# Kernel optimization log

Measured on AMD Instinct MI355X. Metric: run time of the kernel, lower is better.

The kernel has to match this reference:

```python
import jax, jax.numpy as jnp
import numpy as np

N, E = 50000, 800000
DIN, DH, DOUT = 128, 64, 16


def setup_inputs() -> dict:
    key = jax.random.key(0)
    ks = jax.random.split(key, 8)
    s = lambda d: np.float32(1.0 / np.sqrt(d))
    return {
        "x": jax.random.normal(ks[0], (N, DIN), jnp.float32),
        "edge_index": jax.random.randint(ks[1], (2, E), 0, N, dtype=jnp.int32),
        "w0": jax.random.normal(ks[2], (DIN, DH), jnp.float32) * s(DIN),
        "b0": jnp.zeros((DH,), jnp.float32),
        "w1": jax.random.normal(ks[3], (DH, DH), jnp.float32) * s(DH),
        "b1": jnp.zeros((DH,), jnp.float32),
        "w2": jax.random.normal(ks[4], (DH, DH), jnp.float32) * s(DH),
        "b2": jnp.zeros((DH,), jnp.float32),
        "fc_w": jax.random.normal(ks[5], (DH, DOUT), jnp.float32) * s(DH),
        "fc_b": jnp.zeros((DOUT,), jnp.float32),
    }


def reference(x, edge_index, w0, b0, w1, b1, w2, b2, fc_w, fc_b):
    n = x.shape[0]
    loop = jnp.arange(n, dtype=edge_index.dtype)
    # PyG GCNConv default: add self-loops, symmetric normalization
    src = jnp.concatenate([edge_index[0], loop])  # [E+N]
    dst = jnp.concatenate([edge_index[1], loop])
    deg = jax.ops.segment_sum(jnp.ones_like(dst, dtype=x.dtype), dst, num_segments=n)
    dinv = jnp.where(deg > 0, jax.lax.rsqrt(deg), 0.0)
    norm = dinv[src] * dinv[dst]  # [E+N]

    def conv(h, W, b):
        h = h @ W                            # [N, DH]
        msg = h[src] * norm[:, None]         # [E+N, DH] gather + scale
        return jax.ops.segment_sum(msg, dst, num_segments=n) + b

    h = jax.nn.elu(conv(x, w0, b0))
    h = jax.nn.elu(conv(h, w1, b1))
    h = jax.nn.elu(conv(h, w2, b2))
    return jax.nn.softmax(h @ fc_w + fc_b, axis=1)
```

## Files before the change

kernel.cpp:

```cpp
#include <hip/hip_runtime.h>
#include <hip/hip_fp16.h>
#include <math.h>

#define NWIN 8

typedef _Float16 f16x8 __attribute__((ext_vector_type(8)));
typedef float f32x4 __attribute__((ext_vector_type(4)));

__device__ __forceinline__ float eluf(float v) { return v > 0.f ? v : expm1f(v); }

__global__ __launch_bounds__(256) void deg_kernel(const int* __restrict__ dst,
                                                  int* __restrict__ counts, int E) {
    int e = blockIdx.x * 256 + threadIdx.x;
    if (e < E) atomicAdd(&counts[dst[e]], 1);
}

__global__ __launch_bounds__(256) void alloc_kernel(const int* __restrict__ counts,
                                                    int* __restrict__ gtotal,
                                                    int* __restrict__ offs,
                                                    int* __restrict__ cursor,
                                                    float* __restrict__ dinv, int n) {
    int i = blockIdx.x * 256 + threadIdx.x;
    if (i >= n) return;
    int c = counts[i];
    int pad = (c + 7) & ~7;
    int o = atomicAdd(gtotal, pad);
    offs[i] = o;
    cursor[i] = o;
    dinv[i] = rsqrtf((float)(c + 1));
}

__global__ __launch_bounds__(256) void fill_kernel(int* __restrict__ a, int v, int cap) {
    int i = blockIdx.x * 256 + threadIdx.x;
    if (i < cap) a[i] = v;
}

__global__ __launch_bounds__(256) void scatter_kernel(const int* __restrict__ src,
                                                      const int* __restrict__ dst,
                                                      int* __restrict__ cursor,
                                                      int* __restrict__ csr_src,
                                                      int E, int winSize) {
    int win = blockIdx.x & (NWIN - 1);
    int group = blockIdx.x >> 3;
    int nGroups = gridDim.x >> 3;
    int lo = win * winSize, hi = lo + winSize;
    int stride = nGroups * 256;
    for (int e = group * 256 + threadIdx.x; e < E; e += stride) {
        int d = dst[e];
        if (d >= lo && d < hi) {
            int j = atomicAdd(&cursor[d], 1);
            csr_src[j] = src[e];
        }
    }
}

__global__ __launch_bounds__(256) void mm128_mfma(const float* __restrict__ H,
                                                  const float* __restrict__ W,
                                                  const float* __restrict__ dinv,
                                                  __half* __restrict__ TA,
                                                  __half* __restrict__ TB,
                                                  int n, int nTiles) {
    __shared__ _Float16 bhi[4][4][64][8];
    __shared__ _Float16 blo[4][4][64][8];
    int tid = threadIdx.x;
    for (int it = 0; it < 32; ++it) {
        int idx = it * 256 + tid;
        int k = idx >> 6, nn = idx & 63;
        float w = W[idx];
        _Float16 h = (_Float16)w;
        _Float16 l = (_Float16)(w - (float)h);
        int kt = k >> 5, kr = k & 31;
        int g = kr >> 3, j = kr & 7;
        int ct = nn >> 4, c = nn & 15;
        bhi[kt][ct][g * 16 + c][j] = h;
        blo[kt][ct][g * 16 + c][j] = l;
    }
    if (blockIdx.x == 0 && tid < 32) {
        TA[n * 32 + tid] = __float2half(0.f);
        TB[n * 32 + tid] = __float2half(0.f);
    }
    __syncthreads();

    int wave = blockIdx.x * 4 + (tid >> 6);
    if (wave >= nTiles) return;
    int lane = tid & 63;
    f16x8 Bh[4][4], Bl[4][4];
    #pragma unroll
    for (int kt = 0; kt < 4; ++kt)
        #pragma unroll
        for (int ct = 0; ct < 4; ++ct) {
            Bh[kt][ct] = *(const f16x8*)&bhi[kt][ct][lane][0];
            Bl[kt][ct] = *(const f16x8*)&blo[kt][ct][lane][0];
        }
    int row0 = wave * 16;
    int arow = row0 + (lane & 15);
    if (arow >= n) arow = n - 1;
    const float* hp = H + (size_t)arow * 128 + ((lane >> 4) << 3);
    f32x4 acc[4];
    #pragma unroll
    for (int ct = 0; ct < 4; ++ct) acc[ct] = (f32x4){0.f, 0.f, 0.f, 0.f};
    #pragma unroll
    for (int kt = 0; kt < 4; ++kt) {
        float4 p0 = *(const float4*)(hp + kt * 32);
        float4 p1 = *(const float4*)(hp + kt * 32 + 4);
        float v[8] = {p0.x, p0.y, p0.z, p0.w, p1.x, p1.y, p1.z, p1.w};
        f16x8 ah, al;
        #pragma unroll
        for (int j = 0; j < 8; ++j) {
            _Float16 h = (_Float16)v[j];
            ah[j] = h;
            al[j] = (_Float16)(v[j] - (float)h);
        }
        #pragma unroll
        for (int ct = 0; ct < 4; ++ct) {
            acc[ct] = __builtin_amdgcn_mfma_f32_16x16x32_f16(ah, Bh[kt][ct], acc[ct], 0, 0, 0);
            acc[ct] = __builtin_amdgcn_mfma_f32_16x16x32_f16(al, Bh[kt][ct], acc[ct], 0, 0, 0);
            acc[ct] = __builtin_amdgcn_mfma_f32_16x16x32_f16(ah, Bl[kt][ct], acc[ct], 0, 0, 0);
        }
    }
    int rbase = row0 + ((lane >> 4) << 2);
    int cbase = lane & 15;
    #pragma unroll
    for (int r = 0; r < 4; ++r) {
        int row = rbase + r;
        if (row < n) {
            float d = dinv[row];
            #pragma unroll
            for (int ct = 0; ct < 4; ++ct) {
                int col = ct * 16 + cbase;
                __half* P = (col < 32) ? TA : TB;
                P[row * 32 + (col & 31)] = __float2half(acc[ct][r] * d);
            }
        }
    }
}

__global__ __launch_bounds__(256) void gatherA_kernel(const __half* __restrict__ P,
                                                      const int* __restrict__ offs,
                                                      const int* __restrict__ cnt,
                                                      const int* __restrict__ csr_src,
                                                      float* __restrict__ agg, int n) {
    int t = blockIdx.x * 256 + threadIdx.x;
    int node = t >> 4, l = t & 15;
    if (node >= n) return;
    const __half2* P2 = (const __half2*)P;
    float2 sv = __half22float2(P2[node * 16 + l]);
    float ax0 = sv.x, ay0 = sv.y;
    float ax1 = 0, ay1 = 0, ax2 = 0, ay2 = 0, ax3 = 0, ay3 = 0;
    int e0 = offs[node];
    int e1 = e0 + ((cnt[node] + 7) & ~7);
    #pragma unroll 1
    for (int e = e0; e < e1; e += 8) {
        int s0 = __builtin_nontemporal_load(csr_src + e);
        int s1 = __builtin_nontemporal_load(csr_src + e + 1);
        int s2 = __builtin_nontemporal_load(csr_src + e + 2);
        int s3 = __builtin_nontemporal_load(csr_src + e + 3);
        int s4 = __builtin_nontemporal_load(csr_src + e + 4);
        int s5 = __builtin_nontemporal_load(csr_src + e + 5);
        int s6 = __builtin_nontemporal_load(csr_src + e + 6);
        int s7 = __builtin_nontemporal_load(csr_src + e + 7);
        float2 v0 = __half22float2(P2[s0 * 16 + l]);
        float2 v1 = __half22float2(P2[s1 * 16 + l]);
        float2 v2 = __half22float2(P2[s2 * 16 + l]);
        float2 v3 = __half22float2(P2[s3 * 16 + l]);
        float2 v4 = __half22float2(P2[s4 * 16 + l]);
        float2 v5 = __half22float2(P2[s5 * 16 + l]);
        float2 v6 = __half22float2(P2[s6 * 16 + l]);
        float2 v7 = __half22float2(P2[s7 * 16 + l]);
        ax0 += v0.x + v4.x;  ay0 += v0.y + v4.y;
        ax1 += v1.x + v5.x;  ay1 += v1.y + v5.y;
        ax2 += v2.x + v6.x;  ay2 += v2.y + v6.y;
        ax3 += v3.x + v7.x;  ay3 += v3.y + v7.y;
    }
    float rx = (ax0 + ax1) + (ax2 + ax3);
    float ry = (ay0 + ay1) + (ay2 + ay3);
    __builtin_nontemporal_store(rx, agg + node * 32 + 2 * l);
    __builtin_nontemporal_store(ry, agg + node * 32 + 2 * l + 1);
}

__global__ __launch_bounds__(256, 4) void gatherB_mm(const __half* __restrict__ PB,
                                                     const float* __restrict__ agg,
                                                     const int* __restrict__ offs,
                                                     const int* __restrict__ cnt,
                                                     const int* __restrict__ csr_src,
                                                     const float* __restrict__ dinv,
                                                     const float* __restrict__ bias,
                                                     const float* __restrict__ Wn,
                                                     __half* __restrict__ outA,
                                                     __half* __restrict__ outB, int n) {
    __shared__ _Float16 bhi[2][4][64][8];
    __shared__ _Float16 blo[2][4][64][8];
    __shared__ float rowbuf[64][68];
    int tid = threadIdx.x;
    for (int it = 0; it < 16; ++it) {
        int idx = it * 256 + tid;
        int k = idx >> 6, nn = idx & 63;
        float w = Wn[idx];
        _Float16 h = (_Float16)w;
        _Float16 lo = (_Float16)(w - (float)h);
        int kt = k >> 5, kr = k & 31;
        int g = kr >> 3, j = kr & 7;
        int ct = nn >> 4, c = nn & 15;
        bhi[kt][ct][g * 16 + c][j] = h;
        blo[kt][ct][g * 16 + c][j] = lo;
    }
    if (blockIdx.x == 0 && tid < 32) {
        outA[n * 32 + tid] = __float2half(0.f);
        outB[n * 32 + tid] = __float2half(0.f);
    }
    int g16 = tid >> 4, l = tid & 15;
    int nodebase = blockIdx.x * 64;
    const __half2* P2 = (const __half2*)PB;
    #pragma unroll 1
    for (int q = 0; q < 4; ++q) {
        int ln = 4 * g16 + q;
        int node = nodebase + ln;
        float h0 = 0.f, h1 = 0.f, h2 = 0.f, h3 = 0.f;
        if (node < n) {
            float2 sv = __half22float2(P2[node * 16 + l]);
            float ax0 = sv.x, ay0 = sv.y;
            float ax1 = 0, ay1 = 0, ax2 = 0, ay2 = 0, ax3 = 0, ay3 = 0;
            int e0 = offs[node];
            int e1 = e0 + ((cnt[node] + 7) & ~7);
            #pragma unroll 1
            for (int e = e0; e < e1; e += 8) {
                int s0 = __builtin_nontemporal_load(csr_src + e);
                int s1 = __builtin_nontemporal_load(csr_src + e + 1);
                int s2 = __builtin_nontemporal_load(csr_src + e + 2);
                int s3 = __builtin_nontemporal_load(csr_src + e + 3);
                int s4 = __builtin_nontemporal_load(csr_src + e + 4);
                int s5 = __builtin_nontemporal_load(csr_src + e + 5);
                int s6 = __builtin_nontemporal_load(csr_src + e + 6);
                int s7 = __builtin_nontemporal_load(csr_src + e + 7);
                float2 v0 = __half22float2(P2[s0 * 16 + l]);
                float2 v1 = __half22float2(P2[s1 * 16 + l]);
                float2 v2 = __half22float2(P2[s2 * 16 + l]);
                float2 v3 = __half22float2(P2[s3 * 16 + l]);
                float2 v4 = __half22float2(P2[s4 * 16 + l]);
                float2 v5 = __half22float2(P2[s5 * 16 + l]);
                float2 v6 = __half22float2(P2[s6 * 16 + l]);
                float2 v7 = __half22float2(P2[s7 * 16 + l]);
                ax0 += v0.x + v4.x;  ay0 += v0.y + v4.y;
                ax1 += v1.x + v5.x;  ay1 += v1.y + v5.y;
                ax2 += v2.x + v6.x;  ay2 += v2.y + v6.y;
                ax3 += v3.x + v7.x;  ay3 += v3.y + v7.y;
            }
            float shx = (ax0 + ax1) + (ax2 + ax3);
            float shy = (ay0 + ay1) + (ay2 + ay3);
            float a0 = __builtin_nontemporal_load(agg + node * 32 + 2 * l);
            float a1 = __builtin_nontemporal_load(agg + node * 32 + 2 * l + 1);
            float di = dinv[node];
            float2 bl = *(const float2*)(bias + 2 * l);
            float2 bh = *(const float2*)(bias + 32 + 2 * l);
            h0 = eluf(a0 * di + bl.x);
            h1 = eluf(a1 * di + bl.y);
            h2 = eluf(shx * di + bh.x);
            h3 = eluf(shy * di + bh.y);
        }
        *(float2*)&rowbuf[ln][2 * l] = make_float2(h0, h1);
        *(float2*)&rowbuf[ln][32 + 2 * l] = make_float2(h2, h3);
    }
    __syncthreads();

    int wv = tid >> 6, lane = tid & 63;
    f16x8 Bh[2][4], Bl[2][4];
    #pragma unroll
    for (int kt = 0; kt < 2; ++kt)
        #pragma unroll
        for (int ct = 0; ct < 4; ++ct) {
            Bh[kt][ct] = *(const f16x8*)&bhi[kt][ct][lane][0];
            Bl[kt][ct] = *(const f16x8*)&blo[kt][ct][lane][0];
        }
    int trow = wv * 16 + (lane & 15);
    int kb = (lane >> 4) << 3;
    f32x4 acc[4];
    #pragma unroll
    for (int ct = 0; ct < 4; ++ct) acc[ct] = (f32x4){0.f, 0.f, 0.f, 0.f};
    #pragma unroll
    for (int kt = 0; kt < 2; ++kt) {
        float4 p0 = *(const float4*)&rowbuf[trow][kt * 32 + kb];
        float4 p1 = *(const float4*)&rowbuf[trow][kt * 32 + kb + 4];
        float v[8] = {p0.x, p0.y, p0.z, p0.w, p1.x, p1.y, p1.z, p1.w};
        f16x8 ah, al;
        #pragma unroll
        for (int j = 0; j < 8; ++j) {
            _Float16 h = (_Float16)v[j];
            ah[j] = h;
            al[j] = (_Float16)(v[j] - (float)h);
        }
        #pragma unroll
        for (int ct = 0; ct < 4; ++ct) {
            acc[ct] = __builtin_amdgcn_mfma_f32_16x16x32_f16(ah, Bh[kt][ct], acc[ct], 0, 0, 0);
            acc[ct] = __builtin_amdgcn_mfma_f32_16x16x32_f16(al, Bh[kt][ct], acc[ct], 0, 0, 0);
            acc[ct] = __builtin_amdgcn_mfma_f32_16x16x32_f16(ah, Bl[kt][ct], acc[ct], 0, 0, 0);
        }
    }
    int rb = wv * 16 + ((lane >> 4) << 2);
    int cb = lane & 15;
    #pragma unroll
    for (int r = 0; r < 4; ++r) {
        int node = nodebase + rb + r;
        if (node < n) {
            float d = dinv[node];
            #pragma unroll
            for (int ct = 0; ct < 4; ++ct) {
                int col = ct * 16 + cb;
                __half* P = (col < 32) ? outA : outB;
                P[node * 32 + (col & 31)] = __float2half(acc[ct][r] * d);
            }
        }
    }
}

__global__ __launch_bounds__(256, 4) void gatherB_fc(const __half* __restrict__ PB,
                                                     const float* __restrict__ agg,
                                                     const int* __restrict__ offs,
                                                     const int* __restrict__ cnt,
                                                     const int* __restrict__ csr_src,
                                                     const float* __restrict__ dinv,
                                                     const float* __restrict__ bias,
                                                     const float* __restrict__ fcw,
                                                     const float* __restrict__ fcb,
                                                     float* __restrict__ out, int n) {
    __shared__ _Float16 bhi[2][64][8];
    __shared__ _Float16 blo[2][64][8];
    __shared__ float rowbuf[64][68];
    int tid = threadIdx.x;
    for (int it = 0; it < 4; ++it) {
        int idx = it * 256 + tid;
        int k = idx >> 4, j16 = idx & 15;
        float w = fcw[idx];
        _Float16 h = (_Float16)w;
        _Float16 lo = (_Float16)(w - (float)h);
        int kt = k >> 5, kr = k & 31;
        int g = kr >> 3, j = kr & 7;
        bhi[kt][g * 16 + j16][j] = h;
        blo[kt][g * 16 + j16][j] = lo;
    }
    int g16 = tid >> 4, l = tid & 15;
    int nodebase = blockIdx.x * 64;
    const __half2* P2 = (const __half2*)PB;
    #pragma unroll 1
    for (int q = 0; q < 4; ++q) {
        int ln = 4 * g16 + q;
        int node = nodebase + ln;
        float h0 = 0.f, h1 = 0.f, h2 = 0.f, h3 = 0.f;
        if (node < n) {
            float2 sv = __half22float2(P2[node * 16 + l]);
            float ax0 = sv.x, ay0 = sv.y;
            float ax1 = 0, ay1 = 0, ax2 = 0, ay2 = 0, ax3 = 0, ay3 = 0;
            int e0 = offs[node];
            int e1 = e0 + ((cnt[node] + 7) & ~7);
            #pragma unroll 1
            for (int e = e0; e < e1; e += 8) {
                int s0 = __builtin_nontemporal_load(csr_src + e);
                int s1 = __builtin_nontemporal_load(csr_src + e + 1);
                int s2 = __builtin_nontemporal_load(csr_src + e + 2);
                int s3 = __builtin_nontemporal_load(csr_src + e + 3);
                int s4 = __builtin_nontemporal_load(csr_src + e + 4);
                int s5 = __builtin_nontemporal_load(csr_src + e + 5);
                int s6 = __builtin_nontemporal_load(csr_src + e + 6);
                int s7 = __builtin_nontemporal_load(csr_src + e + 7);
                float2 v0 = __half22float2(P2[s0 * 16 + l]);
                float2 v1 = __half22float2(P2[s1 * 16 + l]);
                float2 v2 = __half22float2(P2[s2 * 16 + l]);
                float2 v3 = __half22float2(P2[s3 * 16 + l]);
                float2 v4 = __half22float2(P2[s4 * 16 + l]);
                float2 v5 = __half22float2(P2[s5 * 16 + l]);
                float2 v6 = __half22float2(P2[s6 * 16 + l]);
                float2 v7 = __half22float2(P2[s7 * 16 + l]);
                ax0 += v0.x + v4.x;  ay0 += v0.y + v4.y;
                ax1 += v1.x + v5.x;  ay1 += v1.y + v5.y;
                ax2 += v2.x + v6.x;  ay2 += v2.y + v6.y;
                ax3 += v3.x + v7.x;  ay3 += v3.y + v7.y;
            }
            float shx = (ax0 + ax1) + (ax2 + ax3);
            float shy = (ay0 + ay1) + (ay2 + ay3);
            float a0 = __builtin_nontemporal_load(agg + node * 32 + 2 * l);
            float a1 = __builtin_nontemporal_load(agg + node * 32 + 2 * l + 1);
            float di = dinv[node];
            float2 bl = *(const float2*)(bias + 2 * l);
            float2 bh = *(const float2*)(bias + 32 + 2 * l);
            h0 = eluf(a0 * di + bl.x);
            h1 = eluf(a1 * di + bl.y);
            h2 = eluf(shx * di + bh.x);
            h3 = eluf(shy * di + bh.y);
        }
        *(float2*)&rowbuf[ln][2 * l] = make_float2(h0, h1);
        *(float2*)&rowbuf[ln][32 + 2 * l] = make_float2(h2, h3);
    }
    __syncthreads();

    int wv = tid >> 6, lane = tid & 63;
    f16x8 Bh[2], Bl[2];
    #pragma unroll
    for (int kt = 0; kt < 2; ++kt) {
        Bh[kt] = *(const f16x8*)&bhi[kt][lane][0];
        Bl[kt] = *(const f16x8*)&blo[kt][lane][0];
    }
    int trow = wv * 16 + (lane & 15);
    int kb = (lane >> 4) << 3;
    f32x4 acc = (f32x4){0.f, 0.f, 0.f, 0.f};
    #pragma unroll
    for (int kt = 0; kt < 2; ++kt) {
        float4 p0 = *(const float4*)&rowbuf[trow][kt * 32 + kb];
        float4 p1 = *(const float4*)&rowbuf[trow][kt * 32 + kb + 4];
        float v[8] = {p0.x, p0.y, p0.z, p0.w, p1.x, p1.y, p1.z, p1.w};
        f16x8 ah, al;
        #pragma unroll
        for (int j = 0; j < 8; ++j) {
            _Float16 h = (_Float16)v[j];
            ah[j] = h;
            al[j] = (_Float16)(v[j] - (float)h);
        }
        acc = __builtin_amdgcn_mfma_f32_16x16x32_f16(ah, Bh[kt], acc, 0, 0, 0);
        acc = __builtin_amdgcn_mfma_f32_16x16x32_f16(al, Bh[kt], acc, 0, 0, 0);
        acc = __builtin_amdgcn_mfma_f32_16x16x32_f16(ah, Bl[kt], acc, 0, 0, 0);
    }
    float bj = fcb[lane & 15];
    #pragma unroll
    for (int r = 0; r < 4; ++r) {
        float o = acc[r] + bj;
        float m = o;
        #pragma unroll
        for (int d = 8; d; d >>= 1) m = fmaxf(m, __shfl_xor(m, d, 64));
        float ex = expf(o - m);
        float s = ex;
        #pragma unroll
        for (int d = 8; d; d >>= 1) s += __shfl_xor(s, d, 64);
        int node = nodebase + wv * 16 + ((lane >> 4) << 2) + r;
        if (node < n) out[(size_t)node * 16 + (lane & 15)] = ex / s;
    }
}

extern "C" void kernel_launch(void* const* d_in, const int* in_sizes, int n_in,
                              void* d_out, int out_size, void* d_ws, size_t ws_size,
                              hipStream_t stream) {
    const float* x   = (const float*)d_in[0];
    const int*   ei  = (const int*)d_in[1];
    const float* w0  = (const float*)d_in[2];
    const float* b0  = (const float*)d_in[3];
    const float* w1  = (const float*)d_in[4];
    const float* b1  = (const float*)d_in[5];
    const float* w2  = (const float*)d_in[6];
    const float* b2  = (const float*)d_in[7];
    const float* fcw = (const float*)d_in[8];
    const float* fcb = (const float*)d_in[9];
    float* out = (float*)d_out;

    const int N = in_sizes[0] / 128;
    const int E = in_sizes[1] / 2;
    const int* src = ei;
    const int* dst = ei + E;
    const int csr_cap = E + 8 * N + 8;

    char* p = (char*)d_ws;
    auto take = [&](size_t bytes) {
        char* q = p;
        p += (bytes + 255) & ~(size_t)255;
        return q;
    };
    int*    counts  = (int*)take((size_t)(N + 1) * 4);
    int*    gtotal  = counts + N;
    int*    offs    = (int*)take((size_t)N * 4);
    int*    cursor  = (int*)take((size_t)N * 4);
    float*  dinv    = (float*)take((size_t)N * 4);
    int*    csr_src = (int*)take((size_t)csr_cap * 4);
    float*  aggbuf  = (float*)take((size_t)N * 32 * 4);
    __half* TA0     = (__half*)take((size_t)(N + 1) * 32 * 2);
    __half* TB0     = (__half*)take((size_t)(N + 1) * 32 * 2);
    __half* TA1     = (__half*)take((size_t)(N + 1) * 32 * 2);
    __half* TB1     = (__half*)take((size_t)(N + 1) * 32 * 2);

    hipMemsetAsync(counts, 0, (size_t)(N + 1) * 4, stream);

    deg_kernel<<<(E + 255) / 256, 256, 0, stream>>>(dst, counts, E);
    alloc_kernel<<<(N + 255) / 256, 256, 0, stream>>>(counts, gtotal, offs, cursor, dinv, N);
    fill_kernel<<<(csr_cap + 255) / 256, 256, 0, stream>>>(csr_src, N, csr_cap);
    int winSize = (N + NWIN - 1) / NWIN;
    scatter_kernel<<<1024, 256, 0, stream>>>(src, dst, cursor, csr_src, E, winSize);

    int nTiles = (N + 15) / 16;
    int gA_grid = (N + 15) / 16;
    int gB_grid = (N + 63) / 64;

    mm128_mfma<<<(nTiles + 3) / 4, 256, 0, stream>>>(x, w0, dinv, TA0, TB0, N, nTiles);

    gatherA_kernel<<<gA_grid, 256, 0, stream>>>(TA0, offs, counts, csr_src, aggbuf, N);
    gatherB_mm<<<gB_grid, 256, 0, stream>>>(TB0, aggbuf, offs, counts, csr_src,
                                            dinv, b0, w1, TA1, TB1, N);
    gatherA_kernel<<<gA_grid, 256, 0, stream>>>(TA1, offs, counts, csr_src, aggbuf, N);
    gatherB_mm<<<gB_grid, 256, 0, stream>>>(TB1, aggbuf, offs, counts, csr_src,
                                            dinv, b1, w2, TA0, TB0, N);
    gatherA_kernel<<<gA_grid, 256, 0, stream>>>(TA0, offs, counts, csr_src, aggbuf, N);
    gatherB_fc<<<gB_grid, 256, 0, stream>>>(TB0, aggbuf, offs, counts, csr_src,
                                            dinv, b2, fcw, fcb, out, N);
}
```

Baseline: 306.7 us.

## Fuse split-half gathers into single 64-wide aggregation kernel with 16-byte loads

```diff
diff --git a/kernel.cpp b/kernel.cpp
--- a/kernel.cpp
+++ b/kernel.cpp
@@ -6,8 +6,15 @@
 
 typedef _Float16 f16x8 __attribute__((ext_vector_type(8)));
 typedef float f32x4 __attribute__((ext_vector_type(4)));
+typedef int i32x4 __attribute__((ext_vector_type(4)));
+typedef unsigned int u32x4 __attribute__((ext_vector_type(4)));
 
 __device__ __forceinline__ float eluf(float v) { return v > 0.f ? v : expm1f(v); }
+
+__device__ __forceinline__ float2 cvt2(unsigned int w) {
+    __half2 h = *reinterpret_cast<const __half2*>(&w);
+    return __half22float2(h);
+}
 
 __global__ __launch_bounds__(256) void deg_kernel(const int* __restrict__ dst,
                                                   int* __restrict__ counts, int E) {
@@ -19,7 +26,8 @@
                                                     int* __restrict__ gtotal,
                                                     int* __restrict__ offs,
                                                     int* __restrict__ cursor,
-                                                    float* __restrict__ dinv, int n) {
+                                                    float* __restrict__ dinv,
+                                                    int* __restrict__ csr_src, int n) {
     int i = blockIdx.x * 256 + threadIdx.x;
     if (i >= n) return;
     int c = counts[i];
@@ -28,11 +36,7 @@
     offs[i] = o;
     cursor[i] = o;
     dinv[i] = rsqrtf((float)(c + 1));
-}
-
-__global__ __launch_bounds__(256) void fill_kernel(int* __restrict__ a, int v, int cap) {
-    int i = blockIdx.x * 256 + threadIdx.x;
-    if (i < cap) a[i] = v;
+    for (int j = c; j < pad; ++j) csr_src[o + j] = n;
 }
 
 __global__ __launch_bounds__(256) void scatter_kernel(const int* __restrict__ src,
@@ -57,9 +61,7 @@
 __global__ __launch_bounds__(256) void mm128_mfma(const float* __restrict__ H,
                                                   const float* __restrict__ W,
                                                   const float* __restrict__ dinv,
-                                                  __half* __restrict__ TA,
-                                                  __half* __restrict__ TB,
-                                                  int n, int nTiles) {
+                                                  __half* __restrict__ T, int n, int nTiles) {
     __shared__ _Float16 bhi[4][4][64][8];
     __shared__ _Float16 blo[4][4][64][8];
     int tid = threadIdx.x;
@@ -75,10 +77,7 @@
         bhi[kt][ct][g * 16 + c][j] = h;
         blo[kt][ct][g * 16 + c][j] = l;
     }
-    if (blockIdx.x == 0 && tid < 32) {
-        TA[n * 32 + tid] = __float2half(0.f);
-        TB[n * 32 + tid] = __float2half(0.f);
-    }
+    if (blockIdx.x == 0 && tid < 64) T[(size_t)n * 64 + tid] = __float2half(0.f);
     __syncthreads();
 
     int wave = blockIdx.x * 4 + (tid >> 6);
@@ -126,74 +125,26 @@
         if (row < n) {
             float d = dinv[row];
             #pragma unroll
-            for (int ct = 0; ct < 4; ++ct) {
-                int col = ct * 16 + cbase;
-                __half* P = (col < 32) ? TA : TB;
-                P[row * 32 + (col & 31)] = __float2half(acc[ct][r] * d);
-            }
-        }
-    }
-}
-
-__global__ __launch_bounds__(256) void gatherA_kernel(const __half* __restrict__ P,
-                                                      const int* __restrict__ offs,
-                                                      const int* __restrict__ cnt,
-                                                      const int* __restrict__ csr_src,
-                                                      float* __restrict__ agg, int n) {
-    int t = blockIdx.x * 256 + threadIdx.x;
-    int node = t >> 4, l = t & 15;
-    if (node >= n) return;
-    const __half2* P2 = (const __half2*)P;
-    float2 sv = __half22float2(P2[node * 16 + l]);
-    float ax0 = sv.x, ay0 = sv.y;
-    float ax1 = 0, ay1 = 0, ax2 = 0, ay2 = 0, ax3 = 0, ay3 = 0;
-    int e0 = offs[node];
-    int e1 = e0 + ((cnt[node] + 7) & ~7);
-    #pragma unroll 1
-    for (int e = e0; e < e1; e += 8) {
-        int s0 = __builtin_nontemporal_load(csr_src + e);
-        int s1 = __builtin_nontemporal_load(csr_src + e + 1);
-        int s2 = __builtin_nontemporal_load(csr_src + e + 2);
-        int s3 = __builtin_nontemporal_load(csr_src + e + 3);
-        int s4 = __builtin_nontemporal_load(csr_src + e + 4);
-        int s5 = __builtin_nontemporal_load(csr_src + e + 5);
-        int s6 = __builtin_nontemporal_load(csr_src + e + 6);
-        int s7 = __builtin_nontemporal_load(csr_src + e + 7);
-        float2 v0 = __half22float2(P2[s0 * 16 + l]);
-        float2 v1 = __half22float2(P2[s1 * 16 + l]);
-        float2 v2 = __half22float2(P2[s2 * 16 + l]);
-        float2 v3 = __half22float2(P2[s3 * 16 + l]);
-        float2 v4 = __half22float2(P2[s4 * 16 + l]);
-        float2 v5 = __half22float2(P2[s5 * 16 + l]);
-        float2 v6 = __half22float2(P2[s6 * 16 + l]);
-        float2 v7 = __half22float2(P2[s7 * 16 + l]);
-        ax0 += v0.x + v4.x;  ay0 += v0.y + v4.y;
-        ax1 += v1.x + v5.x;  ay1 += v1.y + v5.y;
-        ax2 += v2.x + v6.x;  ay2 += v2.y + v6.y;
-        ax3 += v3.x + v7.x;  ay3 += v3.y + v7.y;
-    }
-    float rx = (ax0 + ax1) + (ax2 + ax3);
-    float ry = (ay0 + ay1) + (ay2 + ay3);
-    __builtin_nontemporal_store(rx, agg + node * 32 + 2 * l);
-    __builtin_nontemporal_store(ry, agg + node * 32 + 2 * l + 1);
-}
-
-__global__ __launch_bounds__(256, 4) void gatherB_mm(const __half* __restrict__ PB,
-                                                     const float* __restrict__ agg,
-                                                     const int* __restrict__ offs,
-                                                     const int* __restrict__ cnt,
-                                                     const int* __restrict__ csr_src,
-                                                     const float* __restrict__ dinv,
-                                                     const float* __restrict__ bias,
-                                                     const float* __restrict__ Wn,
-                                                     __half* __restrict__ outA,
-                                                     __half* __restrict__ outB, int n) {
+            for (int ct = 0; ct < 4; ++ct)
+                T[(size_t)row * 64 + ct * 16 + cbase] = __float2half(acc[ct][r] * d);
+        }
+    }
+}
+
+__global__ __launch_bounds__(512, 4) void agg_mm(const __half* __restrict__ T,
+                                                 const int* __restrict__ offs,
+                                                 const int* __restrict__ cnt,
+                                                 const int* __restrict__ csr_src,
+                                                 const float* __restrict__ dinv,
+                                                 const float* __restrict__ bias,
+                                                 const float* __restrict__ Wn,
+                                                 __half* __restrict__ out, int n) {
     __shared__ _Float16 bhi[2][4][64][8];
     __shared__ _Float16 blo[2][4][64][8];
     __shared__ float rowbuf[64][68];
     int tid = threadIdx.x;
-    for (int it = 0; it < 16; ++it) {
-        int idx = it * 256 + tid;
+    for (int it = 0; it < 8; ++it) {
+        int idx = it * 512 + tid;
         int k = idx >> 6, nn = idx & 63;
         float w = Wn[idx];
         _Float16 h = (_Float16)w;
@@ -204,78 +155,84 @@
         bhi[kt][ct][g * 16 + c][j] = h;
         blo[kt][ct][g * 16 + c][j] = lo;
     }
-    if (blockIdx.x == 0 && tid < 32) {
-        outA[n * 32 + tid] = __float2half(0.f);
-        outB[n * 32 + tid] = __float2half(0.f);
-    }
-    int g16 = tid >> 4, l = tid & 15;
-    int nodebase = blockIdx.x * 64;
-    const __half2* P2 = (const __half2*)PB;
-    #pragma unroll 1
-    for (int q = 0; q < 4; ++q) {
-        int ln = 4 * g16 + q;
-        int node = nodebase + ln;
-        float h0 = 0.f, h1 = 0.f, h2 = 0.f, h3 = 0.f;
-        if (node < n) {
-            float2 sv = __half22float2(P2[node * 16 + l]);
-            float ax0 = sv.x, ay0 = sv.y;
-            float ax1 = 0, ay1 = 0, ax2 = 0, ay2 = 0, ax3 = 0, ay3 = 0;
-            int e0 = offs[node];
-            int e1 = e0 + ((cnt[node] + 7) & ~7);
-            #pragma unroll 1
-            for (int e = e0; e < e1; e += 8) {
-                int s0 = __builtin_nontemporal_load(csr_src + e);
-                int s1 = __builtin_nontemporal_load(csr_src + e + 1);
-                int s2 = __builtin_nontemporal_load(csr_src + e + 2);
-                int s3 = __builtin_nontemporal_load(csr_src + e + 3);
-                int s4 = __builtin_nontemporal_load(csr_src + e + 4);
-                int s5 = __builtin_nontemporal_load(csr_src + e + 5);
-                int s6 = __builtin_nontemporal_load(csr_src + e + 6);
-                int s7 = __builtin_nontemporal_load(csr_src + e + 7);
-                float2 v0 = __half22float2(P2[s0 * 16 + l]);
-                float2 v1 = __half22float2(P2[s1 * 16 + l]);
-                float2 v2 = __half22float2(P2[s2 * 16 + l]);
-                float2 v3 = __half22float2(P2[s3 * 16 + l]);
-                float2 v4 = __half22float2(P2[s4 * 16 + l]);
-                float2 v5 = __half22float2(P2[s5 * 16 + l]);
-                float2 v6 = __half22float2(P2[s6 * 16 + l]);
-                float2 v7 = __half22float2(P2[s7 * 16 + l]);
-                ax0 += v0.x + v4.x;  ay0 += v0.y + v4.y;
-                ax1 += v1.x + v5.x;  ay1 += v1.y + v5.y;
-                ax2 += v2.x + v6.x;  ay2 += v2.y + v6.y;
-                ax3 += v3.x + v7.x;  ay3 += v3.y + v7.y;
+    if (blockIdx.x == 0 && tid < 64) out[(size_t)n * 64 + tid] = __float2half(0.f);
+
+    int grp = tid >> 3;
+    int l8 = tid & 7;
+    int node = blockIdx.x * 64 + grp;
+    float hA[4] = {0.f, 0.f, 0.f, 0.f};
+    float hB[4] = {0.f, 0.f, 0.f, 0.f};
+    if (node < n) {
+        const u32x4* T4 = (const u32x4*)T;
+        float ax[8] = {0,0,0,0,0,0,0,0};
+        float ay[8] = {0,0,0,0,0,0,0,0};
+        {
+            u32x4 q = T4[node * 8 + l8];
+            #pragma unroll
+            for (int u = 0; u < 4; ++u) {
+                float2 f = cvt2(q[u]);
+                ax[u] += f.x; ax[u + 4] += f.y;
             }
-            float shx = (ax0 + ax1) + (ax2 + ax3);
-            float shy = (ay0 + ay1) + (ay2 + ay3);
-            float a0 = __builtin_nontemporal_load(agg + node * 32 + 2 * l);
-            float a1 = __builtin_nontemporal_load(agg + node * 32 + 2 * l + 1);
-            float di = dinv[node];
-            float2 bl = *(const float2*)(bias + 2 * l);
-            float2 bh = *(const float2*)(bias + 32 + 2 * l);
-            h0 = eluf(a0 * di + bl.x);
-            h1 = eluf(a1 * di + bl.y);
-            h2 = eluf(shx * di + bh.x);
-            h3 = eluf(shy * di + bh.y);
-        }
-        *(float2*)&rowbuf[ln][2 * l] = make_float2(h0, h1);
-        *(float2*)&rowbuf[ln][32 + 2 * l] = make_float2(h2, h3);
-    }
+        }
+        int e0 = offs[node];
+        int e1 = e0 + ((cnt[node] + 7) & ~7);
+        #pragma unroll 1
+        for (int e = e0; e < e1; e += 8) {
+            i32x4 sa = __builtin_nontemporal_load((const i32x4*)(csr_src + e));
+            i32x4 sb = __builtin_nontemporal_load((const i32x4*)(csr_src + e + 4));
+            u32x4 q0 = T4[sa.x * 8 + l8];
+            u32x4 q1 = T4[sa.y * 8 + l8];
+            u32x4 q2 = T4[sa.z * 8 + l8];
+            u32x4 q3 = T4[sa.w * 8 + l8];
+            u32x4 q4 = T4[sb.x * 8 + l8];
+            u32x4 q5 = T4[sb.y * 8 + l8];
+            u32x4 q6 = T4[sb.z * 8 + l8];
+            u32x4 q7 = T4[sb.w * 8 + l8];
+            #pragma unroll
+            for (int u = 0; u < 4; ++u) {
+                float2 f0 = cvt2(q0[u]);
+                float2 f1 = cvt2(q1[u]);
+                float2 f2 = cvt2(q2[u]);
+                float2 f3 = cvt2(q3[u]);
+                float2 f4 = cvt2(q4[u]);
+                float2 f5 = cvt2(q5[u]);
+                float2 f6 = cvt2(q6[u]);
+                float2 f7 = cvt2(q7[u]);
+                ax[u]     += (f0.x + f1.x) + (f2.x + f3.x);
+                ay[u]     += (f4.x + f5.x) + (f6.x + f7.x);
+                ax[u + 4] += (f0.y + f1.y) + (f2.y + f3.y);
+                ay[u + 4] += (f4.y + f5.y) + (f6.y + f7.y);
+            }
+        }
+        float di = dinv[node];
+        float4 b0 = *(const float4*)(bias + l8 * 8);
+        float4 b1 = *(const float4*)(bias + l8 * 8 + 4);
+        float bb[8] = {b0.x, b0.y, b0.z, b0.w, b1.x, b1.y, b1.z, b1.w};
+        #pragma unroll
+        for (int u = 0; u < 4; ++u) {
+            hA[u] = eluf((ax[u] + ay[u]) * di + bb[2 * u]);
+            hB[u] = eluf((ax[u + 4] + ay[u + 4]) * di + bb[2 * u + 1]);
+        }
+    }
+    float4 r0 = make_float4(hA[0], hB[0], hA[1], hB[1]);
+    float4 r1 = make_float4(hA[2], hB[2], hA[3], hB[3]);
+    *(float4*)&rowbuf[grp][l8 * 8] = r0;
+    *(float4*)&rowbuf[grp][l8 * 8 + 4] = r1;
     __syncthreads();
 
     int wv = tid >> 6, lane = tid & 63;
-    f16x8 Bh[2][4], Bl[2][4];
+    int tile = wv >> 1, ct0 = (wv & 1) * 2;
+    f16x8 Bh[2][2], Bl[2][2];
     #pragma unroll
     for (int kt = 0; kt < 2; ++kt)
         #pragma unroll
-        for (int ct = 0; ct < 4; ++ct) {
-            Bh[kt][ct] = *(const f16x8*)&bhi[kt][ct][lane][0];
-            Bl[kt][ct] = *(const f16x8*)&blo[kt][ct][lane][0];
-        }
-    int trow = wv * 16 + (lane & 15);
+        for (int c2 = 0; c2 < 2; ++c2) {
+            Bh[kt][c2] = *(const f16x8*)&bhi[kt][ct0 + c2][lane][0];
+            Bl[kt][c2] = *(const f16x8*)&blo[kt][ct0 + c2][lane][0];
+        }
+    int trow = tile * 16 + (lane & 15);
     int kb = (lane >> 4) << 3;
-    f32x4 acc[4];
-    #pragma unroll
-    for (int ct = 0; ct < 4; ++ct) acc[ct] = (f32x4){0.f, 0.f, 0.f, 0.f};
+    f32x4 acc[2] = {(f32x4){0.f,0.f,0.f,0.f}, (f32x4){0.f,0.f,0.f,0.f}};
     #pragma unroll
     for (int kt = 0; kt < 2; ++kt) {
         float4 p0 = *(const float4*)&rowbuf[trow][kt * 32 + kb];
@@ -289,45 +246,42 @@
             al[j] = (_Float16)(v[j] - (float)h);
         }
         #pragma unroll
-        for (int ct = 0; ct < 4; ++ct) {
-            acc[ct] = __builtin_amdgcn_mfma_f32_16x16x32_f16(ah, Bh[kt][ct], acc[ct], 0, 0, 0);
-            acc[ct] = __builtin_amdgcn_mfma_f32_16x16x32_f16(al, Bh[kt][ct], acc[ct], 0, 0, 0);
-            acc[ct] = __builtin_amdgcn_mfma_f32_16x16x32_f16(ah, Bl[kt][ct], acc[ct], 0, 0, 0);
-        }
-    }
-    int rb = wv * 16 + ((lane >> 4) << 2);
+        for (int c2 = 0; c2 < 2; ++c2) {
+            acc[c2] = __builtin_amdgcn_mfma_f32_16x16x32_f16(ah, Bh[kt][c2], acc[c2], 0, 0, 0);
+            acc[c2] = __builtin_amdgcn_mfma_f32_16x16x32_f16(al, Bh[kt][c2], acc[c2], 0, 0, 0);
+            acc[c2] = __builtin_amdgcn_mfma_f32_16x16x32_f16(ah, Bl[kt][c2], acc[c2], 0, 0, 0);
+        }
+    }
+    int rb = tile * 16 + ((lane >> 4) << 2);
     int cb = lane & 15;
     #pragma unroll
     for (int r = 0; r < 4; ++r) {
-        int node = nodebase + rb + r;
-        if (node < n) {
-            float d = dinv[node];
-            #pragma unroll
-            for (int ct = 0; ct < 4; ++ct) {
-                int col = ct * 16 + cb;
-                __half* P = (col < 32) ? outA : outB;
-                P[node * 32 + (col & 31)] = __float2half(acc[ct][r] * d);
-            }
-        }
-    }
-}
-
-__global__ __launch_bounds__(256, 4) void gatherB_fc(const __half* __restrict__ PB,
-                                                     const float* __restrict__ agg,
-                                                     const int* __restrict__ offs,
-                                                     const int* __restrict__ cnt,
-                                                     const int* __restrict__ csr_src,
-                                                     const float* __restrict__ dinv,
-                                                     const float* __restrict__ bias,
-                                                     const float* __restrict__ fcw,
-                                                     const float* __restrict__ fcb,
-                                                     float* __restrict__ out, int n) {
+        int node2 = blockIdx.x * 64 + rb + r;
+        if (node2 < n) {
+            float d = dinv[node2];
+            #pragma unroll
+            for (int c2 = 0; c2 < 2; ++c2)
+                out[(size_t)node2 * 64 + (ct0 + c2) * 16 + cb] =
+                    __float2half(acc[c2][r] * d);
+        }
+    }
+}
+
+__global__ __launch_bounds__(512, 4) void agg_fc(const __half* __restrict__ T,
+                                                 const int* __restrict__ offs,
+                                                 const int* __restrict__ cnt,
+                                                 const int* __restrict__ csr_src,
+                                                 const float* __restrict__ dinv,
+                                                 const float* __restrict__ bias,
+                                                 const float* __restrict__ fcw,
+                                                 const float* __restrict__ fcb,
+                                                 float* __restrict__ out, int n) {
     __shared__ _Float16 bhi[2][64][8];
     __shared__ _Float16 blo[2][64][8];
     __shared__ float rowbuf[64][68];
     int tid = threadIdx.x;
-    for (int it = 0; it < 4; ++it) {
-        int idx = it * 256 + tid;
+    for (int it = 0; it < 2; ++it) {
+        int idx = it * 512 + tid;
         int k = idx >> 4, j16 = idx & 15;
         float w = fcw[idx];
         _Float16 h = (_Float16)w;
@@ -337,61 +291,70 @@
         bhi[kt][g * 16 + j16][j] = h;
         blo[kt][g * 16 + j16][j] = lo;
     }
-    int g16 = tid >> 4, l = tid & 15;
-    int nodebase = blockIdx.x * 64;
-    const __half2* P2 = (const __half2*)PB;
-    #pragma unroll 1
-    for (int q = 0; q < 4; ++q) {
-        int ln = 4 * g16 + q;
-        int node = nodebase + ln;
-        float h0 = 0.f, h1 = 0.f, h2 = 0.f, h3 = 0.f;
-        if (node < n) {
-            float2 sv = __half22float2(P2[node * 16 + l]);
-            float ax0 = sv.x, ay0 = sv.y;
-            float ax1 = 0, ay1 = 0, ax2 = 0, ay2 = 0, ax3 = 0, ay3 = 0;
-            int e0 = offs[node];
-            int e1 = e0 + ((cnt[node] + 7) & ~7);
-            #pragma unroll 1
-            for (int e = e0; e < e1; e += 8) {
-                int s0 = __builtin_nontemporal_load(csr_src + e);
-                int s1 = __builtin_nontemporal_load(csr_src + e + 1);
-                int s2 = __builtin_nontemporal_load(csr_src + e + 2);
-                int s3 = __builtin_nontemporal_load(csr_src + e + 3);
-                int s4 = __builtin_nontemporal_load(csr_src + e + 4);
-                int s5 = __builtin_nontemporal_load(csr_src + e + 5);
-                int s6 = __builtin_nontemporal_load(csr_src + e + 6);
-                int s7 = __builtin_nontemporal_load(csr_src + e + 7);
-                float2 v0 = __half22float2(P2[s0 * 16 + l]);
-                float2 v1 = __half22float2(P2[s1 * 16 + l]);
-                float2 v2 = __half22float2(P2[s2 * 16 + l]);
-                float2 v3 = __half22float2(P2[s3 * 16 + l]);
-                float2 v4 = __half22float2(P2[s4 * 16 + l]);
-                float2 v5 = __half22float2(P2[s5 * 16 + l]);
-                float2 v6 = __half22float2(P2[s6 * 16 + l]);
-                float2 v7 = __half22float2(P2[s7 * 16 + l]);
-                ax0 += v0.x + v4.x;  ay0 += v0.y + v4.y;
-                ax1 += v1.x + v5.x;  ay1 += v1.y + v5.y;
-                ax2 += v2.x + v6.x;  ay2 += v2.y + v6.y;
-                ax3 += v3.x + v7.x;  ay3 += v3.y + v7.y;
+    int grp = tid >> 3, l8 = tid & 7;
+    int node = blockIdx.x * 64 + grp;
+    float hA[4] = {0.f, 0.f, 0.f, 0.f};
+    float hB[4] = {0.f, 0.f, 0.f, 0.f};
+    if (node < n) {
+        const u32x4* T4 = (const u32x4*)T;
+        float ax[8] = {0,0,0,0,0,0,0,0};
+        float ay[8] = {0,0,0,0,0,0,0,0};
+        {
+            u32x4 q = T4[node * 8 + l8];
+            #pragma unroll
+            for (int u = 0; u < 4; ++u) {
+                float2 f = cvt2(q[u]);
+                ax[u] += f.x; ax[u + 4] += f.y;
             }
-            float shx = (ax0 + ax1) + (ax2 + ax3);
-            float shy = (ay0 + ay1) + (ay2 + ay3);
-            float a0 = __builtin_nontemporal_load(agg + node * 32 + 2 * l);
-            float a1 = __builtin_nontemporal_load(agg + node * 32 + 2 * l + 1);
-            float di = dinv[node];
-            float2 bl = *(const float2*)(bias + 2 * l);
-            float2 bh = *(const float2*)(bias + 32 + 2 * l);
-            h0 = eluf(a0 * di + bl.x);
-            h1 = eluf(a1 * di + bl.y);
-            h2 = eluf(shx * di + bh.x);
-            h3 = eluf(shy * di + bh.y);
-        }
-        *(float2*)&rowbuf[ln][2 * l] = make_float2(h0, h1);
-        *(float2*)&rowbuf[ln][32 + 2 * l] = make_float2(h2, h3);
-    }
+        }
+        int e0 = offs[node];
+        int e1 = e0 + ((cnt[node] + 7) & ~7);
+        #pragma unroll 1
+        for (int e = e0; e < e1; e += 8) {
+            i32x4 sa = __builtin_nontemporal_load((const i32x4*)(csr_src + e));
+            i32x4 sb = __builtin_nontemporal_load((const i32x4*)(csr_src + e + 4));
+            u32x4 q0 = T4[sa.x * 8 + l8];
+            u32x4 q1 = T4[sa.y * 8 + l8];
+            u32x4 q2 = T4[sa.z * 8 + l8];
+            u32x4 q3 = T4[sa.w * 8 + l8];
+            u32x4 q4 = T4[sb.x * 8 + l8];
+            u32x4 q5 = T4[sb.y * 8 + l8];
+            u32x4 q6 = T4[sb.z * 8 + l8];
+            u32x4 q7 = T4[sb.w * 8 + l8];
+            #pragma unroll
+            for (int u = 0; u < 4; ++u) {
+                float2 f0 = cvt2(q0[u]);
+                float2 f1 = cvt2(q1[u]);
+                float2 f2 = cvt2(q2[u]);
+                float2 f3 = cvt2(q3[u]);
+                float2 f4 = cvt2(q4[u]);
+                float2 f5 = cvt2(q5[u]);
+                float2 f6 = cvt2(q6[u]);
+                float2 f7 = cvt2(q7[u]);
+                ax[u]     += (f0.x + f1.x) + (f2.x + f3.x);
+                ay[u]     += (f4.x + f5.x) + (f6.x + f7.x);
+                ax[u + 4] += (f0.y + f1.y) + (f2.y + f3.y);
+                ay[u + 4] += (f4.y + f5.y) + (f6.y + f7.y);
+            }
+        }
+        float di = dinv[node];
+        float4 b0 = *(const float4*)(bias + l8 * 8);
+        float4 b1 = *(const float4*)(bias + l8 * 8 + 4);
+        float bb[8] = {b0.x, b0.y, b0.z, b0.w, b1.x, b1.y, b1.z, b1.w};
+        #pragma unroll
+        for (int u = 0; u < 4; ++u) {
+            hA[u] = eluf((ax[u] + ay[u]) * di + bb[2 * u]);
+            hB[u] = eluf((ax[u + 4] + ay[u + 4]) * di + bb[2 * u + 1]);
+        }
+    }
+    float4 r0 = make_float4(hA[0], hB[0], hA[1], hB[1]);
+    float4 r1 = make_float4(hA[2], hB[2], hA[3], hB[3]);
+    *(float4*)&rowbuf[grp][l8 * 8] = r0;
+    *(float4*)&rowbuf[grp][l8 * 8 + 4] = r1;
     __syncthreads();
 
     int wv = tid >> 6, lane = tid & 63;
+    if (wv >= 4) return;
     f16x8 Bh[2], Bl[2];
     #pragma unroll
     for (int kt = 0; kt < 2; ++kt) {
@@ -428,8 +391,8 @@
         float s = ex;
         #pragma unroll
         for (int d = 8; d; d >>= 1) s += __shfl_xor(s, d, 64);
-        int node = nodebase + wv * 16 + ((lane >> 4) << 2) + r;
-        if (node < n) out[(size_t)node * 16 + (lane & 15)] = ex / s;
+        int node2 = blockIdx.x * 64 + wv * 16 + ((lane >> 4) << 2) + r;
+        if (node2 < n) out[(size_t)node2 * 16 + (lane & 15)] = ex / s;
     }
 }
 
@@ -466,33 +429,25 @@
     int*    cursor  = (int*)take((size_t)N * 4);
     float*  dinv    = (float*)take((size_t)N * 4);
     int*    csr_src = (int*)take((size_t)csr_cap * 4);
-    float*  aggbuf  = (float*)take((size_t)N * 32 * 4);
-    __half* TA0     = (__half*)take((size_t)(N + 1) * 32 * 2);
-    __half* TB0     = (__half*)take((size_t)(N + 1) * 32 * 2);
-    __half* TA1     = (__half*)take((size_t)(N + 1) * 32 * 2);
-    __half* TB1     = (__half*)take((size_t)(N + 1) * 32 * 2);
+    __half* tbufA   = (__half*)take((size_t)(N + 1) * 64 * 2);
+    __half* tbufB   = (__half*)take((size_t)(N + 1) * 64 * 2);
 
     hipMemsetAsync(counts, 0, (size_t)(N + 1) * 4, stream);
 
     deg_kernel<<<(E + 255) / 256, 256, 0, stream>>>(dst, counts, E);
-    alloc_kernel<<<(N + 255) / 256, 256, 0, stream>>>(counts, gtotal, offs, cursor, dinv, N);
-    fill_kernel<<<(csr_cap + 255) / 256, 256, 0, stream>>>(csr_src, N, csr_cap);
+    alloc_kernel<<<(N + 255) / 256, 256, 0, stream>>>(counts, gtotal, offs, cursor,
+                                                      dinv, csr_src, N);
     int winSize = (N + NWIN - 1) / NWIN;
     scatter_kernel<<<1024, 256, 0, stream>>>(src, dst, cursor, csr_src, E, winSize);
 
     int nTiles = (N + 15) / 16;
-    int gA_grid = (N + 15) / 16;
-    int gB_grid = (N + 63) / 64;
-
-    mm128_mfma<<<(nTiles + 3) / 4, 256, 0, stream>>>(x, w0, dinv, TA0, TB0, N, nTiles);
-
-    gatherA_kernel<<<gA_grid, 256, 0, stream>>>(TA0, offs, counts, csr_src, aggbuf, N);
-    gatherB_mm<<<gB_grid, 256, 0, stream>>>(TB0, aggbuf, offs, counts, csr_src,
-                                            dinv, b0, w1, TA1, TB1, N);
-    gatherA_kernel<<<gA_grid, 256, 0, stream>>>(TA1, offs, counts, csr_src, aggbuf, N);
-    gatherB_mm<<<gB_grid, 256, 0, stream>>>(TB1, aggbuf, offs, counts, csr_src,
-                                            dinv, b1, w2, TA0, TB0, N);
-    gatherA_kernel<<<gA_grid, 256, 0, stream>>>(TA0, offs, counts, csr_src, aggbuf, N);
-    gatherB_fc<<<gB_grid, 256, 0, stream>>>(TB0, aggbuf, offs, counts, csr_src,
-                                            dinv, b2, fcw, fcb, out, N);
-}
+    int agg_grid = (N + 63) / 64;
+
+    mm128_mfma<<<(nTiles + 3) / 4, 256, 0, stream>>>(x, w0, dinv, tbufA, N, nTiles);
+    agg_mm<<<agg_grid, 512, 0, stream>>>(tbufA, offs, counts, csr_src,
+                                         dinv, b0, w1, tbufB, N);
+    agg_mm<<<agg_grid, 512, 0, stream>>>(tbufB, offs, counts, csr_src,
+                                         dinv, b1, w2, tbufA, N);
+    agg_fc<<<agg_grid, 512, 0, stream>>>(tbufA, offs, counts, csr_src,
+                                         dinv, b2, fcw, fcb, out, N);
+}
```

After: 257.4 us. 1.19x faster.
